# Optimization experiments

Measured on AMD Instinct MI355X. Metric: run time of the kernel, lower is better.

Reference implementation:

```python
import jax, jax.numpy as jnp
import numpy as np

HEIGHT = 108
WIDTH = 108
LEN_CLASSES = 7
EPS = 1e-5


def layout_bbox(pred, H, W):
    # pred: [B, O, 4 + LEN_CLASSES]
    bbox = pred[..., :4]
    cls_prob = pred[..., 4:]  # [B,O,7]
    x_c = bbox[..., 0] * W   # [B,O]
    y_c = bbox[..., 1] * H
    w = bbox[..., 2] * W
    h = bbox[..., 3] * H
    x1 = (x_c - 0.5 * w)[:, :, None, None]  # [B,O,1,1]
    x2 = (x_c + 0.5 * w)[:, :, None, None]
    y1 = (y_c - 0.5 * h)[:, :, None, None]
    y2 = (y_c + 0.5 * h)[:, :, None, None]
    xt = jnp.arange(W, dtype=pred.dtype)[None, None, None, :]  # [1,1,1,W]
    yt = jnp.arange(H, dtype=pred.dtype)[None, None, :, None]  # [1,1,H,1]
    x1d = xt - x1  # [B,O,1,W]
    x2d = x2 - xt
    y1d = yt - y1  # [B,O,H,1]
    y2d = y2 - yt
    # min(relu(d), 1) == clip(d, 0, 1)
    yband = jnp.clip(y1d, 0.0, 1.0) * jnp.clip(y2d, 0.0, 1.0)  # [B,O,H,1]
    xband = jnp.clip(x1d, 0.0, 1.0) * jnp.clip(x2d, 0.0, 1.0)  # [B,O,1,W]
    x1_line = jax.nn.relu(1.0 - jnp.abs(x1d)) * yband  # [B,O,H,W]
    x2_line = jax.nn.relu(1.0 - jnp.abs(x2d)) * yband
    y1_line = jax.nn.relu(1.0 - jnp.abs(y1d)) * xband
    y2_line = jax.nn.relu(1.0 - jnp.abs(y2d)) * xband
    xy_max = jnp.maximum(jnp.maximum(x1_line, x2_line), jnp.maximum(y1_line, y2_line))  # [B,O,H,W]
    spatial = xy_max[..., None] * cls_prob[:, :, None, None, :]  # [B,O,H,W,7]
    return jnp.max(spatial, axis=1)  # [B,H,W,7]


def bn(x, g, b, axes):
    m = jnp.mean(x, axis=axes, keepdims=True)
    v = jnp.var(x, axis=axes, keepdims=True)
    shape = [1] * x.ndim
    shape[1 if x.ndim == 4 else -1] = -1
    return (x - m) * jax.lax.rsqrt(v + EPS) * g.reshape(shape) + b.reshape(shape)


def conv2d(x, w, b, stride):
    y = jax.lax.conv_general_dilated(x, w, (stride, stride), 'VALID',
                                     dimension_numbers=('NCHW', 'OIHW', 'NCHW'))
    return y + b[None, :, None, None]


def setup_inputs() -> dict:
    key = jax.random.key(0)
    ks = jax.random.split(key, 16)
    B, O = 64, 16
    d = {}
    d['image'] = jax.random.uniform(ks[0], (B, O, 4 + LEN_CLASSES), dtype=jnp.float32)
    d['conv1_w'] = jax.random.normal(ks[1], (32, LEN_CLASSES, 5, 5), jnp.float32) * 0.05
    d['conv1_b'] = jnp.zeros((32,), jnp.float32)
    d['bn1_g'] = jnp.ones((32,), jnp.float32)
    d['bn1_b'] = jnp.zeros((32,), jnp.float32)
    d['conv2_w'] = jax.random.normal(ks[2], (64, 32, 5, 5), jnp.float32) * 0.03
    d['conv2_b'] = jnp.zeros((64,), jnp.float32)
    d['bn2_g'] = jnp.ones((64,), jnp.float32)
    d['bn2_b'] = jnp.zeros((64,), jnp.float32)
    d['fc1_w'] = jax.random.normal(ks[3], (512, 36864), jnp.float32) * 0.005
    d['fc1_b'] = jnp.zeros((512,), jnp.float32)
    d['bn3_g'] = jnp.ones((512,), jnp.float32)
    d['bn3_b'] = jnp.zeros((512,), jnp.float32)
    d['fc2_w'] = jax.random.normal(ks[4], (1, 512), jnp.float32) * 0.04
    d['fc2_b'] = jnp.zeros((1,), jnp.float32)
    return d


def reference(image, conv1_w, conv1_b, bn1_g, bn1_b, conv2_w, conv2_b, bn2_g, bn2_b,
              fc1_w, fc1_b, bn3_g, bn3_b, fc2_w, fc2_b):
    # layout_bbox(image, WIDTH, HEIGHT): output_height=WIDTH, output_width=HEIGHT (both 108)
    layout = layout_bbox(image, WIDTH, HEIGHT)           # [B,108,108,7]
    x = jnp.transpose(layout, (0, 3, 1, 2))              # [B,7,108,108]
    x = conv2d(x, conv1_w, conv1_b, 2)                   # [B,32,52,52]
    x = bn(x, bn1_g, bn1_b, (0, 2, 3))
    x = jax.nn.leaky_relu(x, 0.2)
    x = conv2d(x, conv2_w, conv2_b, 2)                   # [B,64,24,24]
    x = bn(x, bn2_g, bn2_b, (0, 2, 3))
    x = jax.nn.leaky_relu(x, 0.2)
    x = x.reshape(x.shape[0], -1)                        # [B,36864]
    x = x @ fc1_w.T + fc1_b                              # [B,512]
    x = bn(x, bn3_g, bn3_b, (0,))
    x = jax.nn.leaky_relu(x, 0.2)
    x = x @ fc2_w.T + fc2_b                              # [B,1]
    return jax.nn.sigmoid(x)
```

## Files before the change

kernel.cpp:

```cpp
#include <hip/hip_runtime.h>
#include <hip/hip_bf16.h>


typedef unsigned short u16;
typedef __attribute__((ext_vector_type(8))) short bf8_t;
typedef __attribute__((ext_vector_type(4))) float f4_t;
#define MFMA16(a, b, c) __builtin_amdgcn_mfma_f32_16x16x32_bf16(a, b, c, 0, 0, 0)

#define LEAKY(v) (fmaxf((v), 0.2f * (v)))
#define CLIP01(v) fminf(fmaxf((v), 0.0f), 1.0f)

__device__ inline unsigned f2bf(float f) {
  unsigned u = __float_as_uint(f);
  return (u + 0x7FFFu + ((u >> 16) & 1u)) >> 16;
}
__device__ inline float bf2f(unsigned u) { return __uint_as_float(u << 16); }

constexpr int HW = 108;
constexpr int NOBJ = 16;
constexpr int NCLS = 7;

__global__ __launch_bounds__(128) void layout_prep_kernel(
    const float* __restrict__ image, const float* __restrict__ w1,
    const float* __restrict__ w2, u16* __restrict__ lay8,
    u16* __restrict__ wB1, u16* __restrict__ wB2, float* __restrict__ st) {
  int h = blockIdx.x, b = blockIdx.y;
  int tid = threadIdx.x;
  int bid = b * 108 + h;
  if (bid < 114) {
#pragma unroll
    for (int j = 0; j < 4; ++j) {
      int i = bid * 512 + j * 128 + tid;
      if (i < 1216) st[i] = 0.f;
      if (i < 7168) {
        int co = i / 224, k = i % 224;
        int chunk = k >> 5, kk = k & 31, tl = kk >> 3, ci = kk & 7;
        int tap = chunk * 4 + tl;
        unsigned v = 0;
        if (tap < 25 && ci < 7) v = f2bf(w1[co * 175 + ci * 25 + tap]);
        wB1[i] = (u16)v;
      } else if (i < 58368) {
        int jj = i - 7168;
        int tap = jj / 2048, r = jj % 2048, co = r >> 5, ci = r & 31;
        wB2[jj] = (u16)f2bf(w2[co * 800 + ci * 25 + tap]);
      }
    }
  }
  __shared__ float sIm[NOBJ * 11];
  for (int i = tid; i < NOBJ * 11; i += 128) sIm[i] = image[b * NOBJ * 11 + i];
  __syncthreads();
  int w = tid;
  if (w >= HW) return;
  float best[NCLS];
#pragma unroll
  for (int c = 0; c < NCLS; ++c) best[c] = 0.0f;
  float fw = (float)w, fh = (float)h;
  for (int o = 0; o < NOBJ; ++o) {
    const float* p = &sIm[o * 11];
    float xc = p[0] * 108.0f, yc = p[1] * 108.0f;
    float wd = p[2] * 108.0f, hd = p[3] * 108.0f;
    float x1 = xc - 0.5f * wd, x2 = xc + 0.5f * wd;
    float y1 = yc - 0.5f * hd, y2 = yc + 0.5f * hd;
    float x1d = fw - x1, x2d = x2 - fw;
    float y1d = fh - y1, y2d = y2 - fh;
    float yband = CLIP01(y1d) * CLIP01(y2d);
    float xband = CLIP01(x1d) * CLIP01(x2d);
    float x1l = fmaxf(1.0f - fabsf(x1d), 0.0f) * yband;
    float x2l = fmaxf(1.0f - fabsf(x2d), 0.0f) * yband;
    float y1l = fmaxf(1.0f - fabsf(y1d), 0.0f) * xband;
    float y2l = fmaxf(1.0f - fabsf(y2d), 0.0f) * xband;
    float xy = fmaxf(fmaxf(x1l, x2l), fmaxf(y1l, y2l));
#pragma unroll
    for (int c = 0; c < NCLS; ++c) best[c] = fmaxf(best[c], xy * p[4 + c]);
  }
  unsigned p0 = f2bf(best[0]) | (f2bf(best[1]) << 16);
  unsigned p1 = f2bf(best[2]) | (f2bf(best[3]) << 16);
  unsigned p2 = f2bf(best[4]) | (f2bf(best[5]) << 16);
  unsigned p3 = f2bf(best[6]);
  uint4 stv = {p0, p1, p2, p3};
  ((uint4*)lay8)[b * 11664 + h * 108 + w] = stv;
}

__global__ __launch_bounds__(128) void conv1_mfma(
    const u16* __restrict__ lay8, const u16* __restrict__ wB1,
    u16* __restrict__ x1r, float* __restrict__ bn1sum,
    float* __restrict__ bn1sq) {
  int mtg = blockIdx.x, bg = blockIdx.y;
  int tid = threadIdx.x;
  int lane = tid & 63, wv = tid >> 6;
  int f = lane & 15, q = lane >> 4;
  int b = bg * 2 + wv;
  int pbase[4];
  bool mvalid[4];
#pragma unroll
  for (int t = 0; t < 4; ++t) {
    int mt = mtg * 4 + t;
    mvalid[t] = mt < 169;
    int P = min(mt * 16 + f, 2703);
    int oh = P / 52, ow = P - oh * 52;
    pbase[t] = (oh * 2 * 108 + ow * 2) * 8;
  }
  f4_t acc[2][4];
#pragma unroll
  for (int nt = 0; nt < 2; ++nt)
#pragma unroll
    for (int t = 0; t < 4; ++t) acc[nt][t] = {0.f, 0.f, 0.f, 0.f};
  const u16* lb = lay8 + (size_t)b * 93312;
#pragma unroll
  for (int chunk = 0; chunk < 7; ++chunk) {
    int tap = chunk * 4 + q;
    tap = tap > 24 ? 24 : tap;
    int kh = tap / 5, kw = tap - kh * 5;
    int toff = (kh * 108 + kw) * 8;
    bf8_t bf0 = *(const bf8_t*)&wB1[f * 224 + chunk * 32 + q * 8];
    bf8_t bf1 = *(const bf8_t*)&wB1[(16 + f) * 224 + chunk * 32 + q * 8];
#pragma unroll
    for (int t = 0; t < 4; ++t) {
      bf8_t af = *(const bf8_t*)&lb[pbase[t] + toff];
      acc[0][t] = MFMA16(af, bf0, acc[0][t]);
      acc[1][t] = MFMA16(af, bf1, acc[1][t]);
    }
  }
  float s[2] = {0.f, 0.f}, sq[2] = {0.f, 0.f};
  u16* ob = x1r + (size_t)b * 86528;
#pragma unroll
  for (int t = 0; t < 4; ++t) {
    if (!mvalid[t]) continue;
    int P0 = (mtg * 4 + t) * 16 + q * 4;
#pragma unroll
    for (int nt = 0; nt < 2; ++nt)
#pragma unroll
      for (int r = 0; r < 4; ++r) {
        float v = acc[nt][t][r];
        s[nt] += v;
        sq[nt] += v * v;
        ob[(P0 + r) * 32 + nt * 16 + f] = (u16)f2bf(v);
      }
  }
#pragma unroll
  for (int nt = 0; nt < 2; ++nt) {
    s[nt] += __shfl_xor(s[nt], 16);
    s[nt] += __shfl_xor(s[nt], 32);
    sq[nt] += __shfl_xor(sq[nt], 16);
    sq[nt] += __shfl_xor(sq[nt], 32);
  }
  __shared__ float rs[2][32], rq[2][32];
  if (lane < 16) {
#pragma unroll
    for (int nt = 0; nt < 2; ++nt) {
      rs[wv][nt * 16 + f] = s[nt];
      rq[wv][nt * 16 + f] = sq[nt];
    }
  }
  __syncthreads();
  if (tid < 32) {
    atomicAdd(&bn1sum[tid], rs[0][tid] + rs[1][tid]);
    atomicAdd(&bn1sq[tid], rq[0][tid] + rq[1][tid]);
  }
}

__global__ __launch_bounds__(256) void bnapply1_kernel(
    const u16* __restrict__ x1r, const float* __restrict__ bn1sum,
    const float* __restrict__ bn1sq, const float* __restrict__ g1,
    const float* __restrict__ b1, u16* __restrict__ x1b) {
  int idx = blockIdx.x * 256 + threadIdx.x;
  int base = idx * 8, c0 = base & 31;
  float sc[8], sh[8];
#pragma unroll
  for (int j = 0; j < 8; ++j) {
    int c = c0 + j;
    float mean = bn1sum[c] * (1.f / 173056.f);
    float var = bn1sq[c] * (1.f / 173056.f) - mean * mean;
    float s = g1[c] * rsqrtf(var + 1e-5f);
    sc[j] = s;
    sh[j] = b1[c] - mean * s;
  }
  uint4 in = *(const uint4*)&x1r[base];
  unsigned w[4] = {in.x, in.y, in.z, in.w};
  unsigned out[4];
#pragma unroll
  for (int j = 0; j < 4; ++j) {
    float a = bf2f(w[j] & 0xffffu);
    float bq = bf2f(w[j] >> 16);
    a = LEAKY(fmaf(a, sc[2 * j], sh[2 * j]));
    bq = LEAKY(fmaf(bq, sc[2 * j + 1], sh[2 * j + 1]));
    out[j] = f2bf(a) | (f2bf(bq) << 16);
  }
  uint4 stv = {out[0], out[1], out[2], out[3]};
  *(uint4*)&x1b[base] = stv;
}

__global__ __launch_bounds__(256) void conv2_mfma(
    const u16* __restrict__ x1b, const u16* __restrict__ wB2,
    u16* __restrict__ x2b, float* __restrict__ bn2sum,
    float* __restrict__ bn2sq) {
  int mt = blockIdx.x, ntg = blockIdx.y, bz = blockIdx.z;
  int tid = threadIdx.x;
  int lane = tid & 63, wv = tid >> 6;
  int f = lane & 15, q = lane >> 4;
  int co0 = ntg * 32;
  int b0 = bz * 8 + wv * 2;
  int P = mt * 16 + f;
  int oh = P / 24, ow = P - oh * 24;
  int abase = (oh * 2 * 52 + ow * 2) * 32 + q * 8;
  f4_t acc[2][2];
#pragma unroll
  for (int b2 = 0; b2 < 2; ++b2)
#pragma unroll
    for (int n = 0; n < 2; ++n) acc[b2][n] = {0.f, 0.f, 0.f, 0.f};
#pragma unroll
  for (int tap = 0; tap < 25; ++tap) {
    int kh = tap / 5, kw = tap - kh * 5;
    int toff = (kh * 52 + kw) * 32;
    bf8_t bf0 = *(const bf8_t*)&wB2[tap * 2048 + (co0 + f) * 32 + q * 8];
    bf8_t bf1 = *(const bf8_t*)&wB2[tap * 2048 + (co0 + 16 + f) * 32 + q * 8];
#pragma unroll
    for (int b2 = 0; b2 < 2; ++b2) {
      bf8_t af =
          *(const bf8_t*)&x1b[(size_t)(b0 + b2) * 86528 + abase + toff];
      acc[b2][0] = MFMA16(af, bf0, acc[b2][0]);
      acc[b2][1] = MFMA16(af, bf1, acc[b2][1]);
    }
  }
  float s[2] = {0.f, 0.f}, sq[2] = {0.f, 0.f};
#pragma unroll
  for (int b2 = 0; b2 < 2; ++b2) {
    u16* ob = x2b + (size_t)(b0 + b2) * 36864;
#pragma unroll
    for (int n = 0; n < 2; ++n)
#pragma unroll
      for (int r = 0; r < 4; ++r) {
        float v = acc[b2][n][r];
        s[n] += v;
        sq[n] += v * v;
        ob[(mt * 16 + q * 4 + r) * 64 + co0 + n * 16 + f] = (u16)f2bf(v);
      }
  }
#pragma unroll
  for (int n = 0; n < 2; ++n) {
    s[n] += __shfl_xor(s[n], 16);
    s[n] += __shfl_xor(s[n], 32);
    sq[n] += __shfl_xor(sq[n], 16);
    sq[n] += __shfl_xor(sq[n], 32);
  }
  __shared__ float rs[4][32], rq[4][32];
  if (lane < 16) {
#pragma unroll
    for (int n = 0; n < 2; ++n) {
      rs[wv][n * 16 + f] = s[n];
      rq[wv][n * 16 + f] = sq[n];
    }
  }
  __syncthreads();
  if (tid < 32) {
    atomicAdd(&bn2sum[co0 + tid],
              rs[0][tid] + rs[1][tid] + rs[2][tid] + rs[3][tid]);
    atomicAdd(&bn2sq[co0 + tid],
              rq[0][tid] + rq[1][tid] + rq[2][tid] + rq[3][tid]);
  }
}

__global__ __launch_bounds__(256) void bnapply2t_kernel(
    const u16* __restrict__ x2b, const float* __restrict__ bn2sum,
    const float* __restrict__ bn2sq, const float* __restrict__ g2,
    const float* __restrict__ b2, u16* __restrict__ xB) {
  int hw0 = blockIdx.x * 64, b = blockIdx.y;
  __shared__ float tile[64 * 65];
  int t = threadIdx.x;
  int c = t & 63, hl4 = t >> 6;
  float mean = bn2sum[c] * (1.f / 36864.f);
  float var = bn2sq[c] * (1.f / 36864.f) - mean * mean;
  float s = g2[c] * rsqrtf(var + 1e-5f);
  float h = b2[c] - mean * s;
#pragma unroll
  for (int it = 0; it < 16; ++it) {
    int hl = it * 4 + hl4;
    float v = bf2f((unsigned)x2b[((size_t)b * 576 + hw0 + hl) * 64 + c]);
    tile[hl * 65 + c] = LEAKY(fmaf(v, s, h));
  }
  __syncthreads();
  int hw = t & 63, cl4 = t >> 6;
#pragma unroll
  for (int it = 0; it < 16; ++it) {
    int cc = it * 4 + cl4;
    xB[(size_t)b * 36864 + cc * 576 + hw0 + hw] = (u16)f2bf(tile[hw * 65 + cc]);
  }
}

__global__ __launch_bounds__(256) void fc1_mfma(
    const u16* __restrict__ xB, const float* __restrict__ wgt,
    float* __restrict__ part) {
  int ks = blockIdx.x, nb = blockIdx.y;
  int tid = threadIdx.x;
  int lane = tid & 63, wv = tid >> 6;
  int f = lane & 15, q = lane >> 4;
  int n0 = nb * 64 + wv * 16;
  int kbase = ks * 512;
  __shared__ u16 sA[64 * 520];
#pragma unroll
  for (int i = 0; i < 16; ++i) {
    int c = i * 256 + tid;
    int row = c >> 6, col = c & 63;
    *(uint4*)&sA[row * 520 + col * 8] =
        *(const uint4*)&xB[(size_t)row * 36864 + kbase + col * 8];
  }
  __syncthreads();
  f4_t acc[4];
#pragma unroll
  for (int m = 0; m < 4; ++m) acc[m] = {0.f, 0.f, 0.f, 0.f};
  const float* wrow = wgt + (size_t)(n0 + f) * 36864 + kbase + q * 8;
#pragma unroll 4
  for (int kt = 0; kt < 16; ++kt) {
    const float* wp = wrow + kt * 32;
    float4 wa = *(const float4*)wp;
    float4 wb = *(const float4*)(wp + 4);
    union { bf8_t v; u16 u[8]; } bu;
    bu.u[0] = (u16)f2bf(wa.x); bu.u[1] = (u16)f2bf(wa.y);
    bu.u[2] = (u16)f2bf(wa.z); bu.u[3] = (u16)f2bf(wa.w);
    bu.u[4] = (u16)f2bf(wb.x); bu.u[5] = (u16)f2bf(wb.y);
    bu.u[6] = (u16)f2bf(wb.z); bu.u[7] = (u16)f2bf(wb.w);
    bf8_t afr[4];
#pragma unroll
    for (int m = 0; m < 4; ++m)
      afr[m] = *(const bf8_t*)&sA[(m * 16 + f) * 520 + kt * 32 + q * 8];
#pragma unroll
    for (int m = 0; m < 4; ++m) acc[m] = MFMA16(afr[m], bu.v, acc[m]);
  }
  float* pp = part + (size_t)ks * 32768;
#pragma unroll
  for (int m = 0; m < 4; ++m)
#pragma unroll
    for (int r = 0; r < 4; ++r)
      pp[(m * 16 + q * 4 + r) * 512 + n0 + f] = acc[m][r];
}

__global__ __launch_bounds__(128) void fc1_reduce_kernel(
    const float* __restrict__ part, float* __restrict__ fc1o,
    float* __restrict__ bn3sum, float* __restrict__ bn3sq) {
  int i = blockIdx.x * 128 + threadIdx.x;
  float s = 0.f;
#pragma unroll 8
  for (int ks = 0; ks < 72; ++ks) s += part[(size_t)ks * 32768 + i];
  fc1o[i] = s;
  atomicAdd(&bn3sum[i & 511], s);
  atomicAdd(&bn3sq[i & 511], s * s);
}

__global__ __launch_bounds__(64) void fc2_kernel(
    const float* __restrict__ fc1o, const float* __restrict__ bn3sum,
    const float* __restrict__ bn3sq, const float* __restrict__ g3,
    const float* __restrict__ b3, const float* __restrict__ w2,
    const float* __restrict__ b2o, float* __restrict__ out) {
  int m = blockIdx.x;
  int fl = threadIdx.x;
  float a = 0.f;
#pragma unroll
  for (int j = 0; j < 8; ++j) {
    int ff = fl + j * 64;
    float mean = bn3sum[ff] * (1.f / 64.f);
    float var = bn3sq[ff] * (1.f / 64.f) - mean * mean;
    float sc = g3[ff] * rsqrtf(var + 1e-5f);
    float sh = b3[ff] - mean * sc;
    float v = LEAKY(fmaf(fc1o[m * 512 + ff], sc, sh));
    a += v * w2[ff];
  }
  for (int off = 32; off; off >>= 1) a += __shfl_down(a, off, 64);
  if (fl == 0) out[m] = 1.f / (1.f + expf(-(a + b2o[0])));
}

extern "C" void kernel_launch(void* const* d_in, const int* in_sizes, int n_in,
                              void* d_out, int out_size, void* d_ws,
                              size_t ws_size, hipStream_t stream) {
  const float* image = (const float*)d_in[0];
  const float* c1w = (const float*)d_in[1];
  const float* bn1g = (const float*)d_in[3];
  const float* bn1b = (const float*)d_in[4];
  const float* c2w = (const float*)d_in[5];
  const float* bn2g = (const float*)d_in[7];
  const float* bn2b = (const float*)d_in[8];
  const float* f1w = (const float*)d_in[9];
  const float* bn3g = (const float*)d_in[11];
  const float* bn3b = (const float*)d_in[12];
  const float* f2w = (const float*)d_in[13];
  const float* f2b = (const float*)d_in[14];
  float* ws = (float*)d_ws;

  u16* lay8 = (u16*)ws;
  u16* x1r = (u16*)(ws + 2985984);
  u16* x1b = (u16*)(ws + 5754880);
  u16* x2b = (u16*)(ws + 8523776);
  u16* xB = (u16*)(ws + 9703424);
  float* fc1part = ws + 10883072;
  float* fc1o = ws + 13242368;
  float* st = ws + 13275136;
  float* bn1sum = st, *bn1sq = st + 32;
  float* bn2sum = st + 64, *bn2sq = st + 128;
  float* bn3sum = st + 192, *bn3sq = st + 704;
  u16* wB1 = (u16*)(ws + 13276352);
  u16* wB2 = (u16*)(ws + 13279936);

  layout_prep_kernel<<<dim3(108, 64), 128, 0, stream>>>(image, c1w, c2w, lay8,
                                                        wB1, wB2, st);
  conv1_mfma<<<dim3(43, 32), 128, 0, stream>>>(lay8, wB1, x1r, bn1sum, bn1sq);
  bnapply1_kernel<<<2704, 256, 0, stream>>>(x1r, bn1sum, bn1sq, bn1g, bn1b,
                                            x1b);
  conv2_mfma<<<dim3(36, 2, 8), 256, 0, stream>>>(x1b, wB2, x2b, bn2sum,
                                                 bn2sq);
  bnapply2t_kernel<<<dim3(9, 64), 256, 0, stream>>>(x2b, bn2sum, bn2sq, bn2g,
                                                    bn2b, xB);
  fc1_mfma<<<dim3(72, 8), 256, 0, stream>>>(xB, f1w, fc1part);
  fc1_reduce_kernel<<<256, 128, 0, stream>>>(fc1part, fc1o, bn3sum, bn3sq);
  fc2_kernel<<<64, 64, 0, stream>>>(fc1o, bn3sum, bn3sq, bn3g, bn3b, f2w, f2b,
                                    (float*)d_out);
}
```

Before: 253.9 us.

## Fuse all stages into one persistent kernel with software grid barriers

Replaces the eight separate launches with one persistent grid-stride mega-kernel. Stages are separated by an atomic-counter grid barrier, and the BN1 apply is folded into the conv2 input load, removing the x1b round trip. The fc1 split-K is changed from 72 to 64 slices. This removes launch gaps and one intermediate tensor, but relies on every block being co-resident. The barrier has a timeout guard that could break silently, and each stage now runs with fewer blocks than the original kernels.

```diff
diff --git a/kernel.cpp b/kernel.cpp
--- a/kernel.cpp
+++ b/kernel.cpp
@@ -16,356 +16,355 @@
 }
 __device__ inline float bf2f(unsigned u) { return __uint_as_float(u << 16); }
 
-constexpr int HW = 108;
-constexpr int NOBJ = 16;
-constexpr int NCLS = 7;
-
-__global__ __launch_bounds__(128) void layout_prep_kernel(
+__device__ inline void gbar(unsigned* cnt, unsigned target) {
+  __syncthreads();
+  if (threadIdx.x == 0) {
+    __threadfence();
+    atomicAdd(cnt, 1u);
+    unsigned guard = 0;
+    while (__hip_atomic_load(cnt, __ATOMIC_RELAXED, __HIP_MEMORY_SCOPE_AGENT) <
+           target) {
+      __builtin_amdgcn_s_sleep(8);
+      if (++guard > (1u << 17)) break;
+    }
+  }
+  __syncthreads();
+  __threadfence();
+}
+
+__global__ __launch_bounds__(256) void init_kernel(float* __restrict__ st,
+                                                   unsigned* __restrict__ cnt) {
+  for (int i = threadIdx.x; i < 1216; i += 256) st[i] = 0.f;
+  if (threadIdx.x == 0) *cnt = 0u;
+}
+
+__global__ __launch_bounds__(256, 2) void mega_kernel(
     const float* __restrict__ image, const float* __restrict__ w1,
-    const float* __restrict__ w2, u16* __restrict__ lay8,
-    u16* __restrict__ wB1, u16* __restrict__ wB2, float* __restrict__ st) {
-  int h = blockIdx.x, b = blockIdx.y;
-  int tid = threadIdx.x;
-  int bid = b * 108 + h;
-  if (bid < 114) {
-#pragma unroll
-    for (int j = 0; j < 4; ++j) {
-      int i = bid * 512 + j * 128 + tid;
-      if (i < 1216) st[i] = 0.f;
-      if (i < 7168) {
-        int co = i / 224, k = i % 224;
-        int chunk = k >> 5, kk = k & 31, tl = kk >> 3, ci = kk & 7;
-        int tap = chunk * 4 + tl;
-        unsigned v = 0;
-        if (tap < 25 && ci < 7) v = f2bf(w1[co * 175 + ci * 25 + tap]);
-        wB1[i] = (u16)v;
-      } else if (i < 58368) {
-        int jj = i - 7168;
-        int tap = jj / 2048, r = jj % 2048, co = r >> 5, ci = r & 31;
-        wB2[jj] = (u16)f2bf(w2[co * 800 + ci * 25 + tap]);
-      }
-    }
-  }
-  __shared__ float sIm[NOBJ * 11];
-  for (int i = tid; i < NOBJ * 11; i += 128) sIm[i] = image[b * NOBJ * 11 + i];
-  __syncthreads();
-  int w = tid;
-  if (w >= HW) return;
-  float best[NCLS];
-#pragma unroll
-  for (int c = 0; c < NCLS; ++c) best[c] = 0.0f;
-  float fw = (float)w, fh = (float)h;
-  for (int o = 0; o < NOBJ; ++o) {
-    const float* p = &sIm[o * 11];
-    float xc = p[0] * 108.0f, yc = p[1] * 108.0f;
-    float wd = p[2] * 108.0f, hd = p[3] * 108.0f;
-    float x1 = xc - 0.5f * wd, x2 = xc + 0.5f * wd;
-    float y1 = yc - 0.5f * hd, y2 = yc + 0.5f * hd;
-    float x1d = fw - x1, x2d = x2 - fw;
-    float y1d = fh - y1, y2d = y2 - fh;
-    float yband = CLIP01(y1d) * CLIP01(y2d);
-    float xband = CLIP01(x1d) * CLIP01(x2d);
-    float x1l = fmaxf(1.0f - fabsf(x1d), 0.0f) * yband;
-    float x2l = fmaxf(1.0f - fabsf(x2d), 0.0f) * yband;
-    float y1l = fmaxf(1.0f - fabsf(y1d), 0.0f) * xband;
-    float y2l = fmaxf(1.0f - fabsf(y2d), 0.0f) * xband;
-    float xy = fmaxf(fmaxf(x1l, x2l), fmaxf(y1l, y2l));
-#pragma unroll
-    for (int c = 0; c < NCLS; ++c) best[c] = fmaxf(best[c], xy * p[4 + c]);
-  }
-  unsigned p0 = f2bf(best[0]) | (f2bf(best[1]) << 16);
-  unsigned p1 = f2bf(best[2]) | (f2bf(best[3]) << 16);
-  unsigned p2 = f2bf(best[4]) | (f2bf(best[5]) << 16);
-  unsigned p3 = f2bf(best[6]);
-  uint4 stv = {p0, p1, p2, p3};
-  ((uint4*)lay8)[b * 11664 + h * 108 + w] = stv;
-}
-
-__global__ __launch_bounds__(128) void conv1_mfma(
-    const u16* __restrict__ lay8, const u16* __restrict__ wB1,
-    u16* __restrict__ x1r, float* __restrict__ bn1sum,
-    float* __restrict__ bn1sq) {
-  int mtg = blockIdx.x, bg = blockIdx.y;
-  int tid = threadIdx.x;
-  int lane = tid & 63, wv = tid >> 6;
-  int f = lane & 15, q = lane >> 4;
-  int b = bg * 2 + wv;
-  int pbase[4];
-  bool mvalid[4];
-#pragma unroll
-  for (int t = 0; t < 4; ++t) {
-    int mt = mtg * 4 + t;
-    mvalid[t] = mt < 169;
-    int P = min(mt * 16 + f, 2703);
-    int oh = P / 52, ow = P - oh * 52;
-    pbase[t] = (oh * 2 * 108 + ow * 2) * 8;
-  }
-  f4_t acc[2][4];
-#pragma unroll
-  for (int nt = 0; nt < 2; ++nt)
-#pragma unroll
-    for (int t = 0; t < 4; ++t) acc[nt][t] = {0.f, 0.f, 0.f, 0.f};
-  const u16* lb = lay8 + (size_t)b * 93312;
-#pragma unroll
-  for (int chunk = 0; chunk < 7; ++chunk) {
-    int tap = chunk * 4 + q;
-    tap = tap > 24 ? 24 : tap;
-    int kh = tap / 5, kw = tap - kh * 5;
-    int toff = (kh * 108 + kw) * 8;
-    bf8_t bf0 = *(const bf8_t*)&wB1[f * 224 + chunk * 32 + q * 8];
-    bf8_t bf1 = *(const bf8_t*)&wB1[(16 + f) * 224 + chunk * 32 + q * 8];
-#pragma unroll
-    for (int t = 0; t < 4; ++t) {
-      bf8_t af = *(const bf8_t*)&lb[pbase[t] + toff];
-      acc[0][t] = MFMA16(af, bf0, acc[0][t]);
-      acc[1][t] = MFMA16(af, bf1, acc[1][t]);
-    }
-  }
-  float s[2] = {0.f, 0.f}, sq[2] = {0.f, 0.f};
-  u16* ob = x1r + (size_t)b * 86528;
-#pragma unroll
-  for (int t = 0; t < 4; ++t) {
-    if (!mvalid[t]) continue;
-    int P0 = (mtg * 4 + t) * 16 + q * 4;
-#pragma unroll
-    for (int nt = 0; nt < 2; ++nt)
-#pragma unroll
-      for (int r = 0; r < 4; ++r) {
-        float v = acc[nt][t][r];
-        s[nt] += v;
-        sq[nt] += v * v;
-        ob[(P0 + r) * 32 + nt * 16 + f] = (u16)f2bf(v);
-      }
-  }
-#pragma unroll
-  for (int nt = 0; nt < 2; ++nt) {
-    s[nt] += __shfl_xor(s[nt], 16);
-    s[nt] += __shfl_xor(s[nt], 32);
-    sq[nt] += __shfl_xor(sq[nt], 16);
-    sq[nt] += __shfl_xor(sq[nt], 32);
-  }
-  __shared__ float rs[2][32], rq[2][32];
-  if (lane < 16) {
+    const float* __restrict__ w2, const float* __restrict__ g1,
+    const float* __restrict__ b1, const float* __restrict__ g2,
+    const float* __restrict__ b2, const float* __restrict__ f1w,
+    const float* __restrict__ g3, const float* __restrict__ b3,
+    const float* __restrict__ f2w, const float* __restrict__ f2b,
+    float* __restrict__ out, u16* __restrict__ lay8, u16* __restrict__ x1r,
+    u16* __restrict__ x2b, u16* __restrict__ xB, float* __restrict__ part,
+    float* __restrict__ fc1o, float* __restrict__ st, u16* __restrict__ wB1,
+    u16* __restrict__ wB2, unsigned* __restrict__ cnt) {
+  __shared__ __align__(16) char smem[74752];
+  const int tid = threadIdx.x;
+  const int lane = tid & 63, wv = tid >> 6;
+  const int f = lane & 15, q = lane >> 4;
+  const int G = gridDim.x;
+  const int T = G * 256;
+  const int W = G * 4;
+  const int gtid = blockIdx.x * 256 + tid;
+  const int gwid = blockIdx.x * 4 + wv;
+  unsigned tgt = 0;
+  float* bn1sum = st, *bn1sq = st + 32;
+  float* bn2sum = st + 64, *bn2sq = st + 128;
+  float* bn3sum = st + 192, *bn3sq = st + 704;
+
+  for (int i = gtid; i < 58368; i += T) {
+    if (i < 7168) {
+      int co = i / 224, k = i % 224;
+      int chunk = k >> 5, kk = k & 31, tl = kk >> 3, ci = kk & 7;
+      int tap = chunk * 4 + tl;
+      unsigned v = 0;
+      if (tap < 25 && ci < 7) v = f2bf(w1[co * 175 + ci * 25 + tap]);
+      wB1[i] = (u16)v;
+    } else {
+      int jj = i - 7168;
+      int tap = jj / 2048, r = jj & 2047, co = r >> 5, ci = r & 31;
+      wB2[jj] = (u16)f2bf(w2[co * 800 + ci * 25 + tap]);
+    }
+  }
+  for (int pt = gtid; pt < 746496; pt += T) {
+    int b = pt / 11664, rem = pt - b * 11664;
+    int h = rem / 108, w = rem - h * 108;
+    const float* ib = image + b * 176;
+    float best[7];
+#pragma unroll
+    for (int c = 0; c < 7; ++c) best[c] = 0.f;
+    float fw = (float)w, fh = (float)h;
+    for (int o = 0; o < 16; ++o) {
+      const float* p = ib + o * 11;
+      float xc = p[0] * 108.f, yc = p[1] * 108.f;
+      float wd = p[2] * 108.f, hd = p[3] * 108.f;
+      float x1 = xc - 0.5f * wd, x2 = xc + 0.5f * wd;
+      float y1 = yc - 0.5f * hd, y2 = yc + 0.5f * hd;
+      float x1d = fw - x1, x2d = x2 - fw;
+      float y1d = fh - y1, y2d = y2 - fh;
+      float yb = CLIP01(y1d) * CLIP01(y2d);
+      float xb = CLIP01(x1d) * CLIP01(x2d);
+      float x1l = fmaxf(1.f - fabsf(x1d), 0.f) * yb;
+      float x2l = fmaxf(1.f - fabsf(x2d), 0.f) * yb;
+      float y1l = fmaxf(1.f - fabsf(y1d), 0.f) * xb;
+      float y2l = fmaxf(1.f - fabsf(y2d), 0.f) * xb;
+      float xy = fmaxf(fmaxf(x1l, x2l), fmaxf(y1l, y2l));
+#pragma unroll
+      for (int c = 0; c < 7; ++c) best[c] = fmaxf(best[c], xy * p[4 + c]);
+    }
+    uint4 stv = {f2bf(best[0]) | (f2bf(best[1]) << 16),
+                 f2bf(best[2]) | (f2bf(best[3]) << 16),
+                 f2bf(best[4]) | (f2bf(best[5]) << 16), f2bf(best[6])};
+    ((uint4*)lay8)[pt] = stv;
+  }
+  gbar(cnt, tgt += G);
+
+  {
+    float sA[2] = {0.f, 0.f}, sQ[2] = {0.f, 0.f};
+    for (int it = gwid; it < 2752; it += W) {
+      int mtg = it % 43, b = it / 43;
+      int pbase[4];
+      bool mvalid[4];
+#pragma unroll
+      for (int t = 0; t < 4; ++t) {
+        int mt = mtg * 4 + t;
+        mvalid[t] = mt < 169;
+        int P = min(mt * 16 + f, 2703);
+        int oh = P / 52, ow = P - oh * 52;
+        pbase[t] = (oh * 216 + ow * 2) * 8;
+      }
+      f4_t acc[2][4];
+#pragma unroll
+      for (int nt = 0; nt < 2; ++nt)
+#pragma unroll
+        for (int t = 0; t < 4; ++t) acc[nt][t] = {0.f, 0.f, 0.f, 0.f};
+      const u16* lb = lay8 + (size_t)b * 93312;
+#pragma unroll
+      for (int chunk = 0; chunk < 7; ++chunk) {
+        int tap = chunk * 4 + q;
+        tap = tap > 24 ? 24 : tap;
+        int kh = tap / 5, kw = tap - kh * 5;
+        int toff = (kh * 108 + kw) * 8;
+        bf8_t bf0 = *(const bf8_t*)&wB1[f * 224 + chunk * 32 + q * 8];
+        bf8_t bf1 = *(const bf8_t*)&wB1[(16 + f) * 224 + chunk * 32 + q * 8];
+#pragma unroll
+        for (int t = 0; t < 4; ++t) {
+          bf8_t af = *(const bf8_t*)&lb[pbase[t] + toff];
+          acc[0][t] = MFMA16(af, bf0, acc[0][t]);
+          acc[1][t] = MFMA16(af, bf1, acc[1][t]);
+        }
+      }
+      u16* ob = x1r + (size_t)b * 86528;
+#pragma unroll
+      for (int t = 0; t < 4; ++t) {
+        if (!mvalid[t]) continue;
+        int P0 = (mtg * 4 + t) * 16 + q * 4;
+#pragma unroll
+        for (int nt = 0; nt < 2; ++nt)
+#pragma unroll
+          for (int r = 0; r < 4; ++r) {
+            float v = acc[nt][t][r];
+            sA[nt] += v;
+            sQ[nt] += v * v;
+            ob[(P0 + r) * 32 + nt * 16 + f] = (u16)f2bf(v);
+          }
+      }
+    }
 #pragma unroll
     for (int nt = 0; nt < 2; ++nt) {
-      rs[wv][nt * 16 + f] = s[nt];
-      rq[wv][nt * 16 + f] = sq[nt];
-    }
-  }
-  __syncthreads();
-  if (tid < 32) {
-    atomicAdd(&bn1sum[tid], rs[0][tid] + rs[1][tid]);
-    atomicAdd(&bn1sq[tid], rq[0][tid] + rq[1][tid]);
-  }
-}
-
-__global__ __launch_bounds__(256) void bnapply1_kernel(
-    const u16* __restrict__ x1r, const float* __restrict__ bn1sum,
-    const float* __restrict__ bn1sq, const float* __restrict__ g1,
-    const float* __restrict__ b1, u16* __restrict__ x1b) {
-  int idx = blockIdx.x * 256 + threadIdx.x;
-  int base = idx * 8, c0 = base & 31;
-  float sc[8], sh[8];
-#pragma unroll
-  for (int j = 0; j < 8; ++j) {
-    int c = c0 + j;
-    float mean = bn1sum[c] * (1.f / 173056.f);
-    float var = bn1sq[c] * (1.f / 173056.f) - mean * mean;
-    float s = g1[c] * rsqrtf(var + 1e-5f);
-    sc[j] = s;
-    sh[j] = b1[c] - mean * s;
-  }
-  uint4 in = *(const uint4*)&x1r[base];
-  unsigned w[4] = {in.x, in.y, in.z, in.w};
-  unsigned out[4];
-#pragma unroll
-  for (int j = 0; j < 4; ++j) {
-    float a = bf2f(w[j] & 0xffffu);
-    float bq = bf2f(w[j] >> 16);
-    a = LEAKY(fmaf(a, sc[2 * j], sh[2 * j]));
-    bq = LEAKY(fmaf(bq, sc[2 * j + 1], sh[2 * j + 1]));
-    out[j] = f2bf(a) | (f2bf(bq) << 16);
-  }
-  uint4 stv = {out[0], out[1], out[2], out[3]};
-  *(uint4*)&x1b[base] = stv;
-}
-
-__global__ __launch_bounds__(256) void conv2_mfma(
-    const u16* __restrict__ x1b, const u16* __restrict__ wB2,
-    u16* __restrict__ x2b, float* __restrict__ bn2sum,
-    float* __restrict__ bn2sq) {
-  int mt = blockIdx.x, ntg = blockIdx.y, bz = blockIdx.z;
-  int tid = threadIdx.x;
-  int lane = tid & 63, wv = tid >> 6;
-  int f = lane & 15, q = lane >> 4;
-  int co0 = ntg * 32;
-  int b0 = bz * 8 + wv * 2;
-  int P = mt * 16 + f;
-  int oh = P / 24, ow = P - oh * 24;
-  int abase = (oh * 2 * 52 + ow * 2) * 32 + q * 8;
-  f4_t acc[2][2];
-#pragma unroll
-  for (int b2 = 0; b2 < 2; ++b2)
-#pragma unroll
-    for (int n = 0; n < 2; ++n) acc[b2][n] = {0.f, 0.f, 0.f, 0.f};
-#pragma unroll
-  for (int tap = 0; tap < 25; ++tap) {
-    int kh = tap / 5, kw = tap - kh * 5;
-    int toff = (kh * 52 + kw) * 32;
-    bf8_t bf0 = *(const bf8_t*)&wB2[tap * 2048 + (co0 + f) * 32 + q * 8];
-    bf8_t bf1 = *(const bf8_t*)&wB2[tap * 2048 + (co0 + 16 + f) * 32 + q * 8];
-#pragma unroll
-    for (int b2 = 0; b2 < 2; ++b2) {
-      bf8_t af =
-          *(const bf8_t*)&x1b[(size_t)(b0 + b2) * 86528 + abase + toff];
-      acc[b2][0] = MFMA16(af, bf0, acc[b2][0]);
-      acc[b2][1] = MFMA16(af, bf1, acc[b2][1]);
-    }
-  }
-  float s[2] = {0.f, 0.f}, sq[2] = {0.f, 0.f};
-#pragma unroll
-  for (int b2 = 0; b2 < 2; ++b2) {
-    u16* ob = x2b + (size_t)(b0 + b2) * 36864;
-#pragma unroll
-    for (int n = 0; n < 2; ++n)
-#pragma unroll
-      for (int r = 0; r < 4; ++r) {
-        float v = acc[b2][n][r];
-        s[n] += v;
-        sq[n] += v * v;
-        ob[(mt * 16 + q * 4 + r) * 64 + co0 + n * 16 + f] = (u16)f2bf(v);
-      }
-  }
-#pragma unroll
-  for (int n = 0; n < 2; ++n) {
-    s[n] += __shfl_xor(s[n], 16);
-    s[n] += __shfl_xor(s[n], 32);
-    sq[n] += __shfl_xor(sq[n], 16);
-    sq[n] += __shfl_xor(sq[n], 32);
-  }
-  __shared__ float rs[4][32], rq[4][32];
-  if (lane < 16) {
-#pragma unroll
-    for (int n = 0; n < 2; ++n) {
-      rs[wv][n * 16 + f] = s[n];
-      rq[wv][n * 16 + f] = sq[n];
-    }
-  }
-  __syncthreads();
-  if (tid < 32) {
-    atomicAdd(&bn2sum[co0 + tid],
-              rs[0][tid] + rs[1][tid] + rs[2][tid] + rs[3][tid]);
-    atomicAdd(&bn2sq[co0 + tid],
-              rq[0][tid] + rq[1][tid] + rq[2][tid] + rq[3][tid]);
-  }
-}
-
-__global__ __launch_bounds__(256) void bnapply2t_kernel(
-    const u16* __restrict__ x2b, const float* __restrict__ bn2sum,
-    const float* __restrict__ bn2sq, const float* __restrict__ g2,
-    const float* __restrict__ b2, u16* __restrict__ xB) {
-  int hw0 = blockIdx.x * 64, b = blockIdx.y;
-  __shared__ float tile[64 * 65];
-  int t = threadIdx.x;
-  int c = t & 63, hl4 = t >> 6;
-  float mean = bn2sum[c] * (1.f / 36864.f);
-  float var = bn2sq[c] * (1.f / 36864.f) - mean * mean;
-  float s = g2[c] * rsqrtf(var + 1e-5f);
-  float h = b2[c] - mean * s;
-#pragma unroll
-  for (int it = 0; it < 16; ++it) {
-    int hl = it * 4 + hl4;
-    float v = bf2f((unsigned)x2b[((size_t)b * 576 + hw0 + hl) * 64 + c]);
-    tile[hl * 65 + c] = LEAKY(fmaf(v, s, h));
-  }
-  __syncthreads();
-  int hw = t & 63, cl4 = t >> 6;
-#pragma unroll
-  for (int it = 0; it < 16; ++it) {
-    int cc = it * 4 + cl4;
-    xB[(size_t)b * 36864 + cc * 576 + hw0 + hw] = (u16)f2bf(tile[hw * 65 + cc]);
-  }
-}
-
-__global__ __launch_bounds__(256) void fc1_mfma(
-    const u16* __restrict__ xB, const float* __restrict__ wgt,
-    float* __restrict__ part) {
-  int ks = blockIdx.x, nb = blockIdx.y;
-  int tid = threadIdx.x;
-  int lane = tid & 63, wv = tid >> 6;
-  int f = lane & 15, q = lane >> 4;
-  int n0 = nb * 64 + wv * 16;
-  int kbase = ks * 512;
-  __shared__ u16 sA[64 * 520];
-#pragma unroll
-  for (int i = 0; i < 16; ++i) {
-    int c = i * 256 + tid;
-    int row = c >> 6, col = c & 63;
-    *(uint4*)&sA[row * 520 + col * 8] =
-        *(const uint4*)&xB[(size_t)row * 36864 + kbase + col * 8];
-  }
-  __syncthreads();
-  f4_t acc[4];
-#pragma unroll
-  for (int m = 0; m < 4; ++m) acc[m] = {0.f, 0.f, 0.f, 0.f};
-  const float* wrow = wgt + (size_t)(n0 + f) * 36864 + kbase + q * 8;
-#pragma unroll 4
-  for (int kt = 0; kt < 16; ++kt) {
-    const float* wp = wrow + kt * 32;
-    float4 wa = *(const float4*)wp;
-    float4 wb = *(const float4*)(wp + 4);
-    union { bf8_t v; u16 u[8]; } bu;
-    bu.u[0] = (u16)f2bf(wa.x); bu.u[1] = (u16)f2bf(wa.y);
-    bu.u[2] = (u16)f2bf(wa.z); bu.u[3] = (u16)f2bf(wa.w);
-    bu.u[4] = (u16)f2bf(wb.x); bu.u[5] = (u16)f2bf(wb.y);
-    bu.u[6] = (u16)f2bf(wb.z); bu.u[7] = (u16)f2bf(wb.w);
-    bf8_t afr[4];
-#pragma unroll
-    for (int m = 0; m < 4; ++m)
-      afr[m] = *(const bf8_t*)&sA[(m * 16 + f) * 520 + kt * 32 + q * 8];
-#pragma unroll
-    for (int m = 0; m < 4; ++m) acc[m] = MFMA16(afr[m], bu.v, acc[m]);
-  }
-  float* pp = part + (size_t)ks * 32768;
-#pragma unroll
-  for (int m = 0; m < 4; ++m)
-#pragma unroll
-    for (int r = 0; r < 4; ++r)
-      pp[(m * 16 + q * 4 + r) * 512 + n0 + f] = acc[m][r];
-}
-
-__global__ __launch_bounds__(128) void fc1_reduce_kernel(
-    const float* __restrict__ part, float* __restrict__ fc1o,
-    float* __restrict__ bn3sum, float* __restrict__ bn3sq) {
-  int i = blockIdx.x * 128 + threadIdx.x;
-  float s = 0.f;
+      sA[nt] += __shfl_xor(sA[nt], 16);
+      sA[nt] += __shfl_xor(sA[nt], 32);
+      sQ[nt] += __shfl_xor(sQ[nt], 16);
+      sQ[nt] += __shfl_xor(sQ[nt], 32);
+    }
+    float* rs = (float*)smem;
+    float* rq = rs + 128;
+    if (lane < 16) {
+#pragma unroll
+      for (int nt = 0; nt < 2; ++nt) {
+        rs[wv * 32 + nt * 16 + f] = sA[nt];
+        rq[wv * 32 + nt * 16 + f] = sQ[nt];
+      }
+    }
+    __syncthreads();
+    if (tid < 32) {
+      atomicAdd(&bn1sum[tid],
+                rs[tid] + rs[32 + tid] + rs[64 + tid] + rs[96 + tid]);
+      atomicAdd(&bn1sq[tid],
+                rq[tid] + rq[32 + tid] + rq[64 + tid] + rq[96 + tid]);
+    }
+  }
+  gbar(cnt, tgt += G);
+
+  {
+    float sc1[8], sh1[8];
+#pragma unroll
+    for (int j = 0; j < 8; ++j) {
+      int c = q * 8 + j;
+      float mean = bn1sum[c] * (1.f / 173056.f);
+      float var = bn1sq[c] * (1.f / 173056.f) - mean * mean;
+      float s = g1[c] * rsqrtf(var + 1e-5f);
+      sc1[j] = s;
+      sh1[j] = b1[c] - mean * s;
+    }
+    float s2[4] = {0.f, 0.f, 0.f, 0.f}, q2[4] = {0.f, 0.f, 0.f, 0.f};
+    for (int it = gwid; it < 2304; it += W) {
+      int mt = it % 36, b = it / 36;
+      int P = mt * 16 + f;
+      int oh = P / 24, ow = P - oh * 24;
+      int abase = (oh * 104 + ow * 2) * 32 + q * 8;
+      const u16* ab = x1r + (size_t)b * 86528;
+      f4_t acc[4];
+#pragma unroll
+      for (int n = 0; n < 4; ++n) acc[n] = {0.f, 0.f, 0.f, 0.f};
+#pragma unroll
+      for (int tap = 0; tap < 25; ++tap) {
+        int kh = tap / 5, kw = tap - kh * 5;
+        int toff = (kh * 52 + kw) * 32;
+        uint4 raw = *(const uint4*)&ab[abase + toff];
+        unsigned wd[4] = {raw.x, raw.y, raw.z, raw.w};
+        union { bf8_t v; u16 u[8]; } r;
+#pragma unroll
+        for (int k2 = 0; k2 < 4; ++k2) {
+          float lo = bf2f(wd[k2] & 0xffffu);
+          float hi = bf2f(wd[k2] >> 16);
+          lo = LEAKY(fmaf(lo, sc1[2 * k2], sh1[2 * k2]));
+          hi = LEAKY(fmaf(hi, sc1[2 * k2 + 1], sh1[2 * k2 + 1]));
+          r.u[2 * k2] = (u16)f2bf(lo);
+          r.u[2 * k2 + 1] = (u16)f2bf(hi);
+        }
+        const u16* wp = &wB2[tap * 2048 + f * 32 + q * 8];
+#pragma unroll
+        for (int n = 0; n < 4; ++n) {
+          bf8_t bf = *(const bf8_t*)&wp[n * 512];
+          acc[n] = MFMA16(r.v, bf, acc[n]);
+        }
+      }
+      u16* ob = x2b + (size_t)b * 36864;
+#pragma unroll
+      for (int n = 0; n < 4; ++n)
+#pragma unroll
+        for (int rr = 0; rr < 4; ++rr) {
+          float v = acc[n][rr];
+          s2[n] += v;
+          q2[n] += v * v;
+          ob[(mt * 16 + q * 4 + rr) * 64 + n * 16 + f] = (u16)f2bf(v);
+        }
+    }
+#pragma unroll
+    for (int n = 0; n < 4; ++n) {
+      s2[n] += __shfl_xor(s2[n], 16);
+      s2[n] += __shfl_xor(s2[n], 32);
+      q2[n] += __shfl_xor(q2[n], 16);
+      q2[n] += __shfl_xor(q2[n], 32);
+    }
+    float* rs = (float*)smem;
+    float* rq = rs + 256;
+    if (lane < 16) {
+#pragma unroll
+      for (int n = 0; n < 4; ++n) {
+        rs[wv * 64 + n * 16 + f] = s2[n];
+        rq[wv * 64 + n * 16 + f] = q2[n];
+      }
+    }
+    __syncthreads();
+    if (tid < 64) {
+      atomicAdd(&bn2sum[tid],
+                rs[tid] + rs[64 + tid] + rs[128 + tid] + rs[192 + tid]);
+      atomicAdd(&bn2sq[tid],
+                rq[tid] + rq[64 + tid] + rq[128 + tid] + rq[192 + tid]);
+    }
+  }
+  gbar(cnt, tgt += G);
+
+  {
+    float* tile = (float*)smem;
+    int c = tid & 63, hl4 = tid >> 6;
+    float mean = bn2sum[c] * (1.f / 36864.f);
+    float var = bn2sq[c] * (1.f / 36864.f) - mean * mean;
+    float s = g2[c] * rsqrtf(var + 1e-5f);
+    float hh = b2[c] - mean * s;
+    for (int vb = blockIdx.x; vb < 576; vb += G) {
+      int hw0 = (vb % 9) * 64, b = vb / 9;
+      __syncthreads();
+#pragma unroll
+      for (int itr = 0; itr < 16; ++itr) {
+        int hl = itr * 4 + hl4;
+        float v = bf2f((unsigned)x2b[((size_t)b * 576 + hw0 + hl) * 64 + c]);
+        tile[hl * 65 + c] = LEAKY(fmaf(v, s, hh));
+      }
+      __syncthreads();
+#pragma unroll
+      for (int itr = 0; itr < 16; ++itr) {
+        int cc = itr * 4 + (tid >> 6);
+        xB[(size_t)b * 36864 + cc * 576 + hw0 + (tid & 63)] =
+            (u16)f2bf(tile[(tid & 63) * 65 + cc]);
+      }
+    }
+  }
+  gbar(cnt, tgt += G);
+
+  {
+    u16* sAr = (u16*)smem;
+    for (int vb = blockIdx.x; vb < 512; vb += G) {
+      int ks = vb >> 3, nb = vb & 7;
+      int n0 = nb * 64 + wv * 16;
+      int kb = ks * 576;
+      __syncthreads();
+      for (int c = tid; c < 4608; c += 256) {
+        int row = c / 72, col = c - row * 72;
+        *(uint4*)&sAr[row * 584 + col * 8] =
+            *(const uint4*)&xB[(size_t)row * 36864 + kb + col * 8];
+      }
+      __syncthreads();
+      f4_t acc[4];
+#pragma unroll
+      for (int m = 0; m < 4; ++m) acc[m] = {0.f, 0.f, 0.f, 0.f};
+      const float* wrow = f1w + (size_t)(n0 + f) * 36864 + kb + q * 8;
+#pragma unroll 3
+      for (int kt = 0; kt < 18; ++kt) {
+        const float* wp = wrow + kt * 32;
+        float4 wa = *(const float4*)wp;
+        float4 wb = *(const float4*)(wp + 4);
+        union { bf8_t v; u16 u[8]; } bu;
+        bu.u[0] = (u16)f2bf(wa.x); bu.u[1] = (u16)f2bf(wa.y);
+        bu.u[2] = (u16)f2bf(wa.z); bu.u[3] = (u16)f2bf(wa.w);
+        bu.u[4] = (u16)f2bf(wb.x); bu.u[5] = (u16)f2bf(wb.y);
+        bu.u[6] = (u16)f2bf(wb.z); bu.u[7] = (u16)f2bf(wb.w);
+        bf8_t afr[4];
+#pragma unroll
+        for (int m = 0; m < 4; ++m)
+          afr[m] = *(const bf8_t*)&sAr[(m * 16 + f) * 584 + kt * 32 + q * 8];
+#pragma unroll
+        for (int m = 0; m < 4; ++m) acc[m] = MFMA16(afr[m], bu.v, acc[m]);
+      }
+      float* pp = part + (size_t)ks * 32768;
+#pragma unroll
+      for (int m = 0; m < 4; ++m)
+#pragma unroll
+        for (int r = 0; r < 4; ++r)
+          pp[(m * 16 + q * 4 + r) * 512 + n0 + f] = acc[m][r];
+    }
+  }
+  gbar(cnt, tgt += G);
+
+  for (int i = gtid; i < 32768; i += T) {
+    float s = 0.f;
 #pragma unroll 8
-  for (int ks = 0; ks < 72; ++ks) s += part[(size_t)ks * 32768 + i];
-  fc1o[i] = s;
-  atomicAdd(&bn3sum[i & 511], s);
-  atomicAdd(&bn3sq[i & 511], s * s);
-}
-
-__global__ __launch_bounds__(64) void fc2_kernel(
-    const float* __restrict__ fc1o, const float* __restrict__ bn3sum,
-    const float* __restrict__ bn3sq, const float* __restrict__ g3,
-    const float* __restrict__ b3, const float* __restrict__ w2,
-    const float* __restrict__ b2o, float* __restrict__ out) {
-  int m = blockIdx.x;
-  int fl = threadIdx.x;
-  float a = 0.f;
-#pragma unroll
-  for (int j = 0; j < 8; ++j) {
-    int ff = fl + j * 64;
-    float mean = bn3sum[ff] * (1.f / 64.f);
-    float var = bn3sq[ff] * (1.f / 64.f) - mean * mean;
-    float sc = g3[ff] * rsqrtf(var + 1e-5f);
-    float sh = b3[ff] - mean * sc;
-    float v = LEAKY(fmaf(fc1o[m * 512 + ff], sc, sh));
-    a += v * w2[ff];
-  }
-  for (int off = 32; off; off >>= 1) a += __shfl_down(a, off, 64);
-  if (fl == 0) out[m] = 1.f / (1.f + expf(-(a + b2o[0])));
+    for (int ks2 = 0; ks2 < 64; ++ks2) s += part[(size_t)ks2 * 32768 + i];
+    fc1o[i] = s;
+    atomicAdd(&bn3sum[i & 511], s);
+    atomicAdd(&bn3sq[i & 511], s * s);
+  }
+  gbar(cnt, tgt += G);
+
+  if (blockIdx.x < 64 && tid < 64) {
+    int m = blockIdx.x;
+    float a = 0.f;
+#pragma unroll
+    for (int j = 0; j < 8; ++j) {
+      int ff = tid + j * 64;
+      float mean = bn3sum[ff] * (1.f / 64.f);
+      float var = bn3sq[ff] * (1.f / 64.f) - mean * mean;
+      float sc = g3[ff] * rsqrtf(var + 1e-5f);
+      float sh = b3[ff] - mean * sc;
+      float v = LEAKY(fmaf(fc1o[m * 512 + ff], sc, sh));
+      a += v * f2w[ff];
+    }
+    for (int off = 32; off; off >>= 1) a += __shfl_down(a, off, 64);
+    if (tid == 0) out[m] = 1.f / (1.f + expf(-(a + f2b[0])));
+  }
 }
 
 extern "C" void kernel_launch(void* const* d_in, const int* in_sizes, int n_in,
@@ -384,32 +383,32 @@
   const float* f2w = (const float*)d_in[13];
   const float* f2b = (const float*)d_in[14];
   float* ws = (float*)d_ws;
+  float* outp = (float*)d_out;
 
   u16* lay8 = (u16*)ws;
   u16* x1r = (u16*)(ws + 2985984);
-  u16* x1b = (u16*)(ws + 5754880);
-  u16* x2b = (u16*)(ws + 8523776);
-  u16* xB = (u16*)(ws + 9703424);
-  float* fc1part = ws + 10883072;
-  float* fc1o = ws + 13242368;
-  float* st = ws + 13275136;
-  float* bn1sum = st, *bn1sq = st + 32;
-  float* bn2sum = st + 64, *bn2sq = st + 128;
-  float* bn3sum = st + 192, *bn3sq = st + 704;
-  u16* wB1 = (u16*)(ws + 13276352);
-  u16* wB2 = (u16*)(ws + 13279936);
-
-  layout_prep_kernel<<<dim3(108, 64), 128, 0, stream>>>(image, c1w, c2w, lay8,
-                                                        wB1, wB2, st);
-  conv1_mfma<<<dim3(43, 32), 128, 0, stream>>>(lay8, wB1, x1r, bn1sum, bn1sq);
-  bnapply1_kernel<<<2704, 256, 0, stream>>>(x1r, bn1sum, bn1sq, bn1g, bn1b,
-                                            x1b);
-  conv2_mfma<<<dim3(36, 2, 8), 256, 0, stream>>>(x1b, wB2, x2b, bn2sum,
-                                                 bn2sq);
-  bnapply2t_kernel<<<dim3(9, 64), 256, 0, stream>>>(x2b, bn2sum, bn2sq, bn2g,
-                                                    bn2b, xB);
-  fc1_mfma<<<dim3(72, 8), 256, 0, stream>>>(xB, f1w, fc1part);
-  fc1_reduce_kernel<<<256, 128, 0, stream>>>(fc1part, fc1o, bn3sum, bn3sq);
-  fc2_kernel<<<64, 64, 0, stream>>>(fc1o, bn3sum, bn3sq, bn3g, bn3b, f2w, f2b,
-                                    (float*)d_out);
+  u16* x2b = (u16*)(ws + 5754880);
+  u16* xB = (u16*)(ws + 6934528);
+  float* part = ws + 8114176;
+  float* fc1o = ws + 10211328;
+  float* st = ws + 10244096;
+  unsigned* cnt = (unsigned*)(ws + 10245312);
+  u16* wB1 = (u16*)(ws + 10245328);
+  u16* wB2 = (u16*)(ws + 10248912);
+
+  static int nblk = 0;
+  if (nblk == 0) {
+    int perCU = 0;
+    hipOccupancyMaxActiveBlocksPerMultiprocessor(
+        &perCU, reinterpret_cast<const void*>(mega_kernel), 256, 0);
+    if (perCU < 1) perCU = 1;
+    if (perCU > 2) perCU = 2;
+    nblk = perCU * 256;
+  }
+
+  init_kernel<<<1, 256, 0, stream>>>(st, cnt);
+  mega_kernel<<<nblk, 256, 0, stream>>>(image, c1w, c2w, bn1g, bn1b, bn2g,
+                                        bn2b, f1w, bn3g, bn3b, f2w, f2b, outp,
+                                        lay8, x1r, x2b, xB, part, fc1o, st,
+                                        wB1, wB2, cnt);
 }
```

Result: slower. 504.1 us (+98.5%).
